# Kernel optimization log

Hardware: AMD Instinct MI355X
Metric: run time of the kernel (lower is better)

Reference implementation:

```python
import jax, jax.numpy as jnp
import numpy as np

NUM_HEADS = 4
IN_CHANNELS = 128


def setup_inputs() -> dict:
    key = jax.random.key(0)
    k_x, k_wq, k_bq, k_wo, k_bo = jax.random.split(key, 5)
    b, c, h, w = 16, IN_CHANNELS, 32, 32
    x = jax.random.normal(k_x, (b, c, h, w), dtype=jnp.float32)
    # 1x1 convs stored as (out_ch, in_ch) matrices
    w_qkv = jax.random.normal(k_wq, (c * 3 * NUM_HEADS, c), dtype=jnp.float32) * 0.02
    b_qkv = jax.random.normal(k_bq, (c * 3 * NUM_HEADS,), dtype=jnp.float32) * 0.02
    w_out = jax.random.normal(k_wo, (c, c * NUM_HEADS), dtype=jnp.float32) * 0.02
    b_out = jax.random.normal(k_bo, (c,), dtype=jnp.float32) * 0.02
    return {"x": x, "w_qkv": w_qkv, "b_qkv": b_qkv, "w_out": w_out, "b_out": b_out}


def reference(x, w_qkv, b_qkv, w_out, b_out):
    b, c, h, w = x.shape
    nh = NUM_HEADS
    # norm is Identity. 1x1 conv == per-pixel matmul over channels.
    qkv = jnp.einsum('bchw,oc->bohw', x, w_qkv) + b_qkv[None, :, None, None]
    qkv = qkv.reshape(b, nh, 3 * c, h, w)
    q, k, v = qkv[:, :, :c], qkv[:, :, c:2 * c], qkv[:, :, 2 * c:]
    # q, v: (b, nh, c, h, w) -> (b*nh, h*w, c); k -> (b*nh, c, h*w)
    q = q.transpose(0, 1, 3, 4, 2).reshape(b * nh, h * w, c)
    k = k.reshape(b * nh, c, h * w)
    v = v.transpose(0, 1, 3, 4, 2).reshape(b * nh, h * w, c)
    scores = jnp.einsum('bnc,bcm->bnm', q, k) * (c ** -0.5)  # (b*nh, hw, hw)
    attn = jax.nn.softmax(scores, axis=-1)
    out = jnp.einsum('bnm,bmc->bnc', attn, v)  # (b*nh, hw, c)
    out = out.reshape(b, nh, h, w, c).transpose(0, 4, 1, 2, 3).reshape(b, nh * c, h, w)
    out = jnp.einsum('bchw,oc->bohw', out, w_out) + b_out[None, :, None, None]
    return out + x
```

## Files before the change

### kernel.cpp

```cpp
#include <hip/hip_runtime.h>
#include <hip/hip_bf16.h>

typedef float  f32x4_v   __attribute__((ext_vector_type(4)));
typedef float  f32x16_v  __attribute__((ext_vector_type(16)));
typedef __bf16 bf16x8_v  __attribute__((ext_vector_type(8)));
typedef __bf16 bf16x4_v  __attribute__((ext_vector_type(4)));

#define WS_Q  0
#define WS_K  8388608
#define WS_V  16777216
#define WS_O  25165824
#define WS_WP 33554432

__device__ __forceinline__ int aswz(int p) { return ((p & 7) ^ ((p >> 3) & 7)) << 4; }

__device__ __forceinline__ void gload16(const void* g, void* l) {
    __builtin_amdgcn_global_load_lds(
        (const __attribute__((address_space(1))) unsigned int*)g,
        (__attribute__((address_space(3))) unsigned int*)l, 16, 0, 0);
}

__global__ __launch_bounds__(256) void k_permute(const float* __restrict__ w_out,
                                                 __bf16* __restrict__ w_perm) {
    int idx  = blockIdx.x * 256 + threadIdx.x;
    int head = idx >> 14;
    int o    = (idx >> 7) & 127;
    int c    = idx & 127;
    w_perm[idx] = (__bf16)w_out[o * 512 + c * 4 + head];
}

__global__ __launch_bounds__(256) void k_qkv(const float* __restrict__ x,
                                             const float* __restrict__ w_qkv,
                                             const float* __restrict__ b_qkv,
                                             __bf16* __restrict__ q_ws,
                                             __bf16* __restrict__ k_ws,
                                             __bf16* __restrict__ v_ws) {
    __shared__ __bf16 Ash[128 * 128];
    __shared__ __bf16 Bsh[128 * 128];
    const int tid = threadIdx.x;
    const int nt  = blockIdx.x;
    const int mt  = blockIdx.y;
    const int gm0 = mt * 128;
    const int b   = gm0 >> 10;
    const int p0  = gm0 & 1023;
    const int o0  = nt * 128;

    char* Ab = reinterpret_cast<char*>(Ash);
    char* Bb = reinterpret_cast<char*>(Bsh);

    for (int it = 0; it < 16; ++it) {
        int idx = tid + it * 256;
        int c   = idx >> 5;
        int i4  = (idx & 31) << 2;
        float4 v = *reinterpret_cast<const float4*>(x + b * 131072 + c * 1024 + p0 + i4);
        float vv[4] = {v.x, v.y, v.z, v.w};
#pragma unroll
        for (int j = 0; j < 4; ++j) {
            int p = i4 + j;
            int byte = ((p << 8) | (c << 1)) ^ aswz(p);
            *reinterpret_cast<__bf16*>(Ab + byte) = (__bf16)vv[j];
        }
    }
    for (int it = 0; it < 16; ++it) {
        int idx = tid + it * 256;
        int o   = idx >> 5;
        int c4  = (idx & 31) << 2;
        float4 v = *reinterpret_cast<const float4*>(w_qkv + (o0 + o) * 128 + c4);
        bf16x4_v h;
        h[0] = (__bf16)v.x; h[1] = (__bf16)v.y; h[2] = (__bf16)v.z; h[3] = (__bf16)v.w;
        int byte = ((o << 8) | (c4 << 1)) ^ aswz(o);
        *reinterpret_cast<bf16x4_v*>(Bb + byte) = h;
    }
    __syncthreads();

    const int lane = tid & 63;
    const int wv   = tid >> 6;
    const int wm   = (wv >> 1) * 64;
    const int wn   = (wv & 1) * 64;
    const int lr   = lane & 15;
    const int lg   = lane >> 4;

    f32x4_v acc[4][4] = {};
#pragma unroll
    for (int ks = 0; ks < 4; ++ks) {
        bf16x8_v af[4], bfr[4];
#pragma unroll
        for (int mi = 0; mi < 4; ++mi) {
            int row  = wm + mi * 16 + lr;
            int byte = ((row << 8) | (ks << 6) | (lg << 4)) ^ aswz(row);
            af[mi] = *reinterpret_cast<const bf16x8_v*>(Ab + byte);
        }
#pragma unroll
        for (int ni = 0; ni < 4; ++ni) {
            int row  = wn + ni * 16 + lr;
            int byte = ((row << 8) | (ks << 6) | (lg << 4)) ^ aswz(row);
            bfr[ni] = *reinterpret_cast<const bf16x8_v*>(Bb + byte);
        }
#pragma unroll
        for (int mi = 0; mi < 4; ++mi)
#pragma unroll
            for (int ni = 0; ni < 4; ++ni)
                acc[mi][ni] = __builtin_amdgcn_mfma_f32_16x16x32_bf16(af[mi], bfr[ni], acc[mi][ni], 0, 0, 0);
    }

#pragma unroll
    for (int ni = 0; ni < 4; ++ni) {
        int o    = o0 + wn + ni * 16 + lr;
        int head = o / 384;
        int rem  = o - head * 384;
        int type = rem >> 7;
        int ch   = rem & 127;
        float bias = b_qkv[o];
        int bh   = (b << 2) + head;
#pragma unroll
        for (int mi = 0; mi < 4; ++mi) {
            int prow = p0 + wm + mi * 16 + lg * 4;
            f32x4_v a = acc[mi][ni];
            if (type == 0) {
#pragma unroll
                for (int r = 0; r < 4; ++r)
                    q_ws[bh * 131072 + (prow + r) * 128 + ch] =
                        (__bf16)((a[r] + bias) * 0.12751744f);
            } else if (type == 1) {
#pragma unroll
                for (int r = 0; r < 4; ++r)
                    k_ws[bh * 131072 + (prow + r) * 128 + ch] = (__bf16)(a[r] + bias);
            } else {
                bf16x4_v hv;
#pragma unroll
                for (int r = 0; r < 4; ++r) hv[r] = (__bf16)(a[r] + bias);
                *reinterpret_cast<bf16x4_v*>(&v_ws[bh * 131072 + ch * 1024 + prow]) = hv;
            }
        }
    }
}

__device__ __forceinline__ void stage_kv(const __bf16* kg, const __bf16* vg,
                                         __bf16* kl, __bf16* vl, int wv, int lane) {
    const int s16 = lane & 15, r4 = lane >> 4;
    const int s8  = lane & 7,  r8 = lane >> 3;
#pragma unroll
    for (int i = 0; i < 4; ++i) {
        int row = wv * 16 + i * 4 + r4;
        const char* src = (const char*)(kg + row * 128) + ((s16 ^ (row & 7)) << 4);
        char* dst = (char*)kl + (wv * 16 + i * 4) * 256;
        gload16(src, dst);
    }
#pragma unroll
    for (int i = 0; i < 4; ++i) {
        int row = wv * 32 + i * 8 + r8;
        const char* src = (const char*)(vg + row * 1024) + ((s8 ^ (row & 7)) << 4);
        char* dst = (char*)vl + (wv * 32 + i * 8) * 128;
        gload16(src, dst);
    }
}

__global__ __launch_bounds__(256, 2) void k_attn(const __bf16* __restrict__ q_ws,
                                                 const __bf16* __restrict__ k_ws,
                                                 const __bf16* __restrict__ v_ws,
                                                 __bf16* __restrict__ o_ws) {
    __shared__ __bf16 Kbuf[2][64 * 128];
    __shared__ __bf16 Vbuf[2][128 * 64];

    const int tid  = threadIdx.x;
    const int lane = tid & 63;
    const int wv   = tid >> 6;
    const int col  = lane & 31;
    const int hi   = lane >> 5;

    const int id   = blockIdx.x;
    const int bh   = (id & 7) * 8 + (id >> 6);
    const int qt   = (id >> 3) & 7;
    const int base = bh * 131072;
    const int q0w  = qt * 128 + wv * 32;

    bf16x8_v bq[8];
    const __bf16* qp = q_ws + base + (q0w + col) * 128 + hi * 8;
#pragma unroll
    for (int ks = 0; ks < 8; ++ks)
        bq[ks] = *reinterpret_cast<const bf16x8_v*>(qp + ks * 16);

    f32x16_v of[4] = {};
    float m = -1e30f, l = 0.f;

    stage_kv(k_ws + base, v_ws + base, &Kbuf[0][0], &Vbuf[0][0], wv, lane);

    for (int t = 0; t < 16; ++t) {
        const int cur = t & 1;
        if (t < 15) {
            stage_kv(k_ws + base + (t + 1) * 64 * 128, v_ws + base + (t + 1) * 64,
                     &Kbuf[cur ^ 1][0], &Vbuf[cur ^ 1][0], wv, lane);
            asm volatile("s_waitcnt vmcnt(8)" ::: "memory");
        } else {
            asm volatile("s_waitcnt vmcnt(0)" ::: "memory");
        }
        __builtin_amdgcn_s_barrier();
        asm volatile("" ::: "memory");
        __builtin_amdgcn_sched_barrier(0);

        const char* Kl = (const char*)&Kbuf[cur][0];
        const char* Vl = (const char*)&Vbuf[cur][0];

        f32x16_v sa = {}, sb = {};
        __builtin_amdgcn_s_setprio(1);
#pragma unroll
        for (int ks = 0; ks < 8; ++ks) {
            const int sl = 2 * ks + hi;
            bf16x8_v af0 = *reinterpret_cast<const bf16x8_v*>(Kl + col * 256 + ((sl ^ (col & 7)) << 4));
            bf16x8_v af1 = *reinterpret_cast<const bf16x8_v*>(Kl + (32 + col) * 256 + ((sl ^ (col & 7)) << 4));
            sa = __builtin_amdgcn_mfma_f32_32x32x16_bf16(af0, bq[ks], sa, 0, 0, 0);
            sb = __builtin_amdgcn_mfma_f32_32x32x16_bf16(af1, bq[ks], sb, 0, 0, 0);
        }
        __builtin_amdgcn_s_setprio(0);

        float v = sa[0];
#pragma unroll
        for (int r = 1; r < 16; ++r) v = fmaxf(v, sa[r]);
#pragma unroll
        for (int r = 0; r < 16; ++r) v = fmaxf(v, sb[r]);
        float pmax = fmaxf(v, __shfl_xor(v, 32));
        if (!__all(pmax - m <= 8.0f)) {
            float fr = __builtin_amdgcn_exp2f(m - pmax);
            m = pmax;
            l *= fr;
#pragma unroll
            for (int r = 0; r < 16; ++r) {
                float frd = __shfl(fr, (r & 3) + 4 * hi + 8 * (r >> 2));
                of[0][r] *= frd; of[1][r] *= frd; of[2][r] *= frd; of[3][r] *= frd;
            }
        }
        float rs = 0.f;
#pragma unroll
        for (int r = 0; r < 16; ++r) { sa[r] = __builtin_amdgcn_exp2f(sa[r] - m); rs += sa[r]; }
#pragma unroll
        for (int r = 0; r < 16; ++r) { sb[r] = __builtin_amdgcn_exp2f(sb[r] - m); rs += sb[r]; }
        l += rs + __shfl_xor(rs, 32);

        bf16x8_v pa[4];
#pragma unroll
        for (int j = 0; j < 4; ++j) {
            const f32x16_v& sj = (j < 2) ? sa : sb;
            const int ro = 8 * (j & 1);
            unsigned w0, w1, w2, w3;
            asm("v_cvt_pk_bf16_f32 %0, %1, %2" : "=v"(w0) : "v"(sj[ro + 0]), "v"(sj[ro + 1]));
            asm("v_cvt_pk_bf16_f32 %0, %1, %2" : "=v"(w2) : "v"(sj[ro + 4]), "v"(sj[ro + 5]));
            asm("v_cvt_pk_bf16_f32 %0, %1, %2" : "=v"(w1) : "v"(sj[ro + 2]), "v"(sj[ro + 3]));
            asm("v_cvt_pk_bf16_f32 %0, %1, %2" : "=v"(w3) : "v"(sj[ro + 6]), "v"(sj[ro + 7]));
            asm("v_permlane32_swap_b32 %0, %1" : "+v"(w0), "+v"(w2));
            asm("v_permlane32_swap_b32 %0, %1" : "+v"(w1), "+v"(w3));
            union { unsigned u[4]; bf16x8_v h; } cvt;
            cvt.u[0] = w0; cvt.u[1] = w1; cvt.u[2] = w2; cvt.u[3] = w3;
            pa[j] = cvt.h;
        }

        __builtin_amdgcn_s_setprio(1);
#pragma unroll
        for (int n = 0; n < 4; ++n) {
#pragma unroll
            for (int j = 0; j < 4; ++j) {
                int row = 32 * n + col;
                bf16x8_v bv = *reinterpret_cast<const bf16x8_v*>(
                    Vl + row * 128 + (((2 * j + hi) ^ (row & 7)) << 4));
                of[n] = __builtin_amdgcn_mfma_f32_32x32x16_bf16(pa[j], bv, of[n], 0, 0, 0);
            }
        }
        __builtin_amdgcn_s_setprio(0);

        asm volatile("s_waitcnt lgkmcnt(0)" ::: "memory");
        __builtin_amdgcn_sched_barrier(0);
        __builtin_amdgcn_s_barrier();
        asm volatile("" ::: "memory");
        __builtin_amdgcn_sched_barrier(0);
    }

    float linv = 1.0f / l;
#pragma unroll
    for (int r = 0; r < 16; ++r) {
        int qr = (r & 3) + 4 * hi + 8 * (r >> 2);
        float ld = __shfl(linv, qr);
        int qg = q0w + qr;
#pragma unroll
        for (int n = 0; n < 4; ++n)
            o_ws[base + qg * 128 + 32 * n + col] = (__bf16)(of[n][r] * ld);
    }
}

__global__ __launch_bounds__(256) void k_out(const __bf16* __restrict__ o_ws,
                                             const __bf16* __restrict__ w_perm,
                                             const float* __restrict__ b_out,
                                             const float* __restrict__ x,
                                             float* __restrict__ out) {
    __shared__ __bf16 Al[64 * 136];
    __shared__ __bf16 Bl[128 * 136];
    const int tid  = threadIdx.x;
    const int lane = tid & 63, wv = tid >> 6;
    const int lr   = lane & 15, lg = lane >> 4;
    const int mt   = blockIdx.x;
    const int gp0  = mt * 64;
    const int b    = gp0 >> 10;
    const int p0   = gp0 & 1023;

    f32x4_v acc[8] = {};
    for (int kc = 0; kc < 4; ++kc) {
        __syncthreads();
#pragma unroll
        for (int it = 0; it < 4; ++it) {
            int idx = tid + it * 256;
            int rr = idx >> 4, k8 = (idx & 15) * 8;
            *reinterpret_cast<bf16x8_v*>(&Al[rr * 136 + k8]) =
                *reinterpret_cast<const bf16x8_v*>(&o_ws[(b * 4 + kc) * 131072 + (p0 + rr) * 128 + k8]);
        }
#pragma unroll
        for (int it = 0; it < 8; ++it) {
            int idx = tid + it * 256;
            int o = idx >> 4, k8 = (idx & 15) * 8;
            *reinterpret_cast<bf16x8_v*>(&Bl[o * 136 + k8]) =
                *reinterpret_cast<const bf16x8_v*>(&w_perm[kc * 16384 + o * 128 + k8]);
        }
        __syncthreads();
#pragma unroll
        for (int ks = 0; ks < 4; ++ks) {
            bf16x8_v af = *reinterpret_cast<const bf16x8_v*>(&Al[(wv * 16 + lr) * 136 + ks * 32 + lg * 8]);
#pragma unroll
            for (int ni = 0; ni < 8; ++ni) {
                bf16x8_v bf_ = *reinterpret_cast<const bf16x8_v*>(&Bl[(ni * 16 + lr) * 136 + ks * 32 + lg * 8]);
                acc[ni] = __builtin_amdgcn_mfma_f32_16x16x32_bf16(af, bf_, acc[ni], 0, 0, 0);
            }
        }
    }

    int prow = p0 + wv * 16 + lg * 4;
#pragma unroll
    for (int ni = 0; ni < 8; ++ni) {
        int o = ni * 16 + lr;
        float bias = b_out[o];
        float4 xr = *reinterpret_cast<const float4*>(&x[b * 131072 + o * 1024 + prow]);
        float4 res;
        res.x = acc[ni][0] + bias + xr.x;
        res.y = acc[ni][1] + bias + xr.y;
        res.z = acc[ni][2] + bias + xr.z;
        res.w = acc[ni][3] + bias + xr.w;
        *reinterpret_cast<float4*>(&out[b * 131072 + o * 1024 + prow]) = res;
    }
}

extern "C" void kernel_launch(void* const* d_in, const int* in_sizes, int n_in,
                              void* d_out, int out_size, void* d_ws, size_t ws_size,
                              hipStream_t stream) {
    const float* x     = (const float*)d_in[0];
    const float* w_qkv = (const float*)d_in[1];
    const float* b_qkv = (const float*)d_in[2];
    const float* w_out = (const float*)d_in[3];
    const float* b_out = (const float*)d_in[4];
    float* out = (float*)d_out;
    __bf16* ws = (__bf16*)d_ws;

    __bf16* q_ws   = ws + WS_Q;
    __bf16* k_ws   = ws + WS_K;
    __bf16* v_ws   = ws + WS_V;
    __bf16* o_ws   = ws + WS_O;
    __bf16* w_perm = ws + WS_WP;

    k_permute<<<256, 256, 0, stream>>>(w_out, w_perm);
    k_qkv<<<dim3(12, 128), 256, 0, stream>>>(x, w_qkv, b_qkv, q_ws, k_ws, v_ws);
    k_attn<<<512, 256, 0, stream>>>(q_ws, k_ws, v_ws, o_ws);
    k_out<<<256, 256, 0, stream>>>(o_ws, w_perm, b_out, x, out);
}
```

Measured before the change: 92.83 us.

## Pre-swizzle Q/K/V into MFMA fragment layout, load V directly to registers

The QKV projection now writes Q, K and V in a layout that matches the MFMA operand fragments, so the attention kernel can load Q and K with contiguous per-lane 16-byte reads and V straight into registers, with no LDS staging for V. Each QKV block now loops over three output tiles, reusing the staged x tile across them, and the weight-permute kernel is folded into the QKV kernel, which removes one launch. The aim is to cut LDS traffic and bank conflicts in attention and to reduce launch and x-reload overhead. In exchange the attention kernel holds more registers for V fragments, and the QKV kernel launches fewer, longer blocks.

```diff
diff --git a/kernel.cpp b/kernel.cpp
--- a/kernel.cpp
+++ b/kernel.cpp
@@ -20,30 +20,30 @@
         (__attribute__((address_space(3))) unsigned int*)l, 16, 0, 0);
 }
 
-__global__ __launch_bounds__(256) void k_permute(const float* __restrict__ w_out,
-                                                 __bf16* __restrict__ w_perm) {
-    int idx  = blockIdx.x * 256 + threadIdx.x;
-    int head = idx >> 14;
-    int o    = (idx >> 7) & 127;
-    int c    = idx & 127;
-    w_perm[idx] = (__bf16)w_out[o * 512 + c * 4 + head];
-}
-
 __global__ __launch_bounds__(256) void k_qkv(const float* __restrict__ x,
                                              const float* __restrict__ w_qkv,
                                              const float* __restrict__ b_qkv,
                                              __bf16* __restrict__ q_ws,
                                              __bf16* __restrict__ k_ws,
-                                             __bf16* __restrict__ v_ws) {
+                                             __bf16* __restrict__ v_ws,
+                                             const float* __restrict__ w_out,
+                                             __bf16* __restrict__ w_perm) {
     __shared__ __bf16 Ash[128 * 128];
     __shared__ __bf16 Bsh[128 * 128];
-    const int tid = threadIdx.x;
-    const int nt  = blockIdx.x;
-    const int mt  = blockIdx.y;
-    const int gm0 = mt * 128;
-    const int b   = gm0 >> 10;
-    const int p0  = gm0 & 1023;
-    const int o0  = nt * 128;
+    const int tid  = threadIdx.x;
+    const int quar = blockIdx.x;
+    const int mt   = blockIdx.y;
+    const int gm0  = mt * 128;
+    const int b    = gm0 >> 10;
+    const int p0   = gm0 & 1023;
+
+    if (quar < 2) {
+        int gid  = (mt * 2 + quar) * 256 + tid;
+        int head = gid >> 14;
+        int o    = (gid >> 7) & 127;
+        int c    = gid & 127;
+        w_perm[gid] = (__bf16)w_out[o * 512 + c * 4 + head];
+    }
 
     char* Ab = reinterpret_cast<char*>(Ash);
     char* Bb = reinterpret_cast<char*>(Bsh);
@@ -61,17 +61,6 @@
             *reinterpret_cast<__bf16*>(Ab + byte) = (__bf16)vv[j];
         }
     }
-    for (int it = 0; it < 16; ++it) {
-        int idx = tid + it * 256;
-        int o   = idx >> 5;
-        int c4  = (idx & 31) << 2;
-        float4 v = *reinterpret_cast<const float4*>(w_qkv + (o0 + o) * 128 + c4);
-        bf16x4_v h;
-        h[0] = (__bf16)v.x; h[1] = (__bf16)v.y; h[2] = (__bf16)v.z; h[3] = (__bf16)v.w;
-        int byte = ((o << 8) | (c4 << 1)) ^ aswz(o);
-        *reinterpret_cast<bf16x4_v*>(Bb + byte) = h;
-    }
-    __syncthreads();
 
     const int lane = tid & 63;
     const int wv   = tid >> 6;
@@ -80,78 +69,85 @@
     const int lr   = lane & 15;
     const int lg   = lane >> 4;
 
-    f32x4_v acc[4][4] = {};
-#pragma unroll
-    for (int ks = 0; ks < 4; ++ks) {
-        bf16x8_v af[4], bfr[4];
-#pragma unroll
-        for (int mi = 0; mi < 4; ++mi) {
-            int row  = wm + mi * 16 + lr;
-            int byte = ((row << 8) | (ks << 6) | (lg << 4)) ^ aswz(row);
-            af[mi] = *reinterpret_cast<const bf16x8_v*>(Ab + byte);
-        }
+    for (int i = 0; i < 3; ++i) {
+        const int o0 = (quar * 3 + i) * 128;
+        __syncthreads();
+        for (int it = 0; it < 16; ++it) {
+            int idx = tid + it * 256;
+            int o   = idx >> 5;
+            int c4  = (idx & 31) << 2;
+            float4 v = *reinterpret_cast<const float4*>(w_qkv + (o0 + o) * 128 + c4);
+            bf16x4_v h;
+            h[0] = (__bf16)v.x; h[1] = (__bf16)v.y; h[2] = (__bf16)v.z; h[3] = (__bf16)v.w;
+            int byte = ((o << 8) | (c4 << 1)) ^ aswz(o);
+            *reinterpret_cast<bf16x4_v*>(Bb + byte) = h;
+        }
+        __syncthreads();
+
+        f32x4_v acc[4][4] = {};
+#pragma unroll
+        for (int ks = 0; ks < 4; ++ks) {
+            bf16x8_v af[4], bfr[4];
+#pragma unroll
+            for (int mi = 0; mi < 4; ++mi) {
+                int row  = wm + mi * 16 + lr;
+                int byte = ((row << 8) | (ks << 6) | (lg << 4)) ^ aswz(row);
+                af[mi] = *reinterpret_cast<const bf16x8_v*>(Ab + byte);
+            }
+#pragma unroll
+            for (int ni = 0; ni < 4; ++ni) {
+                int row  = wn + ni * 16 + lr;
+                int byte = ((row << 8) | (ks << 6) | (lg << 4)) ^ aswz(row);
+                bfr[ni] = *reinterpret_cast<const bf16x8_v*>(Bb + byte);
+            }
+#pragma unroll
+            for (int mi = 0; mi < 4; ++mi)
+#pragma unroll
+                for (int ni = 0; ni < 4; ++ni)
+                    acc[mi][ni] = __builtin_amdgcn_mfma_f32_16x16x32_bf16(af[mi], bfr[ni], acc[mi][ni], 0, 0, 0);
+        }
+
 #pragma unroll
         for (int ni = 0; ni < 4; ++ni) {
-            int row  = wn + ni * 16 + lr;
-            int byte = ((row << 8) | (ks << 6) | (lg << 4)) ^ aswz(row);
-            bfr[ni] = *reinterpret_cast<const bf16x8_v*>(Bb + byte);
-        }
-#pragma unroll
-        for (int mi = 0; mi < 4; ++mi)
-#pragma unroll
-            for (int ni = 0; ni < 4; ++ni)
-                acc[mi][ni] = __builtin_amdgcn_mfma_f32_16x16x32_bf16(af[mi], bfr[ni], acc[mi][ni], 0, 0, 0);
-    }
-
-#pragma unroll
-    for (int ni = 0; ni < 4; ++ni) {
-        int o    = o0 + wn + ni * 16 + lr;
-        int head = o / 384;
-        int rem  = o - head * 384;
-        int type = rem >> 7;
-        int ch   = rem & 127;
-        float bias = b_qkv[o];
-        int bh   = (b << 2) + head;
-#pragma unroll
-        for (int mi = 0; mi < 4; ++mi) {
-            int prow = p0 + wm + mi * 16 + lg * 4;
-            f32x4_v a = acc[mi][ni];
-            if (type == 0) {
-#pragma unroll
-                for (int r = 0; r < 4; ++r)
-                    q_ws[bh * 131072 + (prow + r) * 128 + ch] =
-                        (__bf16)((a[r] + bias) * 0.12751744f);
-            } else if (type == 1) {
-#pragma unroll
-                for (int r = 0; r < 4; ++r)
-                    k_ws[bh * 131072 + (prow + r) * 128 + ch] = (__bf16)(a[r] + bias);
-            } else {
-                bf16x4_v hv;
-#pragma unroll
-                for (int r = 0; r < 4; ++r) hv[r] = (__bf16)(a[r] + bias);
-                *reinterpret_cast<bf16x4_v*>(&v_ws[bh * 131072 + ch * 1024 + prow]) = hv;
-            }
-        }
-    }
-}
-
-__device__ __forceinline__ void stage_kv(const __bf16* kg, const __bf16* vg,
-                                         __bf16* kl, __bf16* vl, int wv, int lane) {
-    const int s16 = lane & 15, r4 = lane >> 4;
-    const int s8  = lane & 7,  r8 = lane >> 3;
-#pragma unroll
-    for (int i = 0; i < 4; ++i) {
-        int row = wv * 16 + i * 4 + r4;
-        const char* src = (const char*)(kg + row * 128) + ((s16 ^ (row & 7)) << 4);
-        char* dst = (char*)kl + (wv * 16 + i * 4) * 256;
-        gload16(src, dst);
-    }
-#pragma unroll
-    for (int i = 0; i < 4; ++i) {
-        int row = wv * 32 + i * 8 + r8;
-        const char* src = (const char*)(vg + row * 1024) + ((s8 ^ (row & 7)) << 4);
-        char* dst = (char*)vl + (wv * 32 + i * 8) * 128;
-        gload16(src, dst);
+            int o    = o0 + wn + ni * 16 + lr;
+            int head = o / 384;
+            int rem  = o - head * 384;
+            int type = rem >> 7;
+            int ch   = rem & 127;
+            float bias = b_qkv[o];
+            int bh   = (b << 2) + head;
+            int ksd  = ch >> 4;
+            int hid  = (ch >> 3) & 1;
+            int ed   = ch & 7;
+#pragma unroll
+            for (int mi = 0; mi < 4; ++mi) {
+                int prow = p0 + wm + mi * 16 + lg * 4;
+                f32x4_v a = acc[mi][ni];
+                if (type == 0) {
+#pragma unroll
+                    for (int r = 0; r < 4; ++r) {
+                        int q = prow + r;
+                        q_ws[bh * 131072 + (q >> 5) * 4096 + ksd * 512 + hid * 256 + (q & 31) * 8 + ed] =
+                            (__bf16)((a[r] + bias) * 0.12751744f);
+                    }
+                } else if (type == 1) {
+#pragma unroll
+                    for (int r = 0; r < 4; ++r) {
+                        int kv = prow + r;
+                        k_ws[bh * 131072 + (kv >> 6) * 8192 + (((kv >> 5) & 1) * 8 + ksd) * 512 +
+                             hid * 256 + (kv & 31) * 8 + ed] = (__bf16)(a[r] + bias);
+                    }
+                } else {
+                    bf16x4_v hv;
+#pragma unroll
+                    for (int r = 0; r < 4; ++r) hv[r] = (__bf16)(a[r] + bias);
+                    int addr = bh * 131072 + (prow >> 6) * 8192 +
+                               ((ch >> 5) * 4 + ((prow >> 4) & 3)) * 512 +
+                               ((prow >> 3) & 1) * 256 + (ch & 31) * 8 + (prow & 7);
+                    *reinterpret_cast<bf16x4_v*>(&v_ws[addr]) = hv;
+                }
+            }
+        }
     }
 }
 
@@ -159,8 +155,7 @@
                                                  const __bf16* __restrict__ k_ws,
                                                  const __bf16* __restrict__ v_ws,
                                                  __bf16* __restrict__ o_ws) {
-    __shared__ __bf16 Kbuf[2][64 * 128];
-    __shared__ __bf16 Vbuf[2][128 * 64];
+    __shared__ __bf16 Kbuf[2][8192];
 
     const int tid  = threadIdx.x;
     const int lane = tid & 63;
@@ -175,50 +170,84 @@
     const int q0w  = qt * 128 + wv * 32;
 
     bf16x8_v bq[8];
-    const __bf16* qp = q_ws + base + (q0w + col) * 128 + hi * 8;
-#pragma unroll
-    for (int ks = 0; ks < 8; ++ks)
-        bq[ks] = *reinterpret_cast<const bf16x8_v*>(qp + ks * 16);
+    {
+        const __bf16* qp = q_ws + base + (q0w >> 5) * 4096 + lane * 8;
+#pragma unroll
+        for (int ks = 0; ks < 8; ++ks)
+            bq[ks] = *reinterpret_cast<const bf16x8_v*>(qp + ks * 512);
+    }
+    asm volatile("s_waitcnt vmcnt(0)" ::: "memory");
+
+    const char* kfb = reinterpret_cast<const char*>(k_ws + base);
+    const uint64_t vfb = (uint64_t)reinterpret_cast<const char*>(v_ws + base) + lane * 16;
+    const int lane16 = lane * 16;
+
+#pragma unroll
+    for (int i = 0; i < 4; ++i)
+        gload16(kfb + (wv * 4 + i) * 1024 + lane16, (char*)&Kbuf[0][0] + (wv * 4 + i) * 1024);
 
     f32x16_v of[4] = {};
     float m = -1e30f, l = 0.f;
-
-    stage_kv(k_ws + base, v_ws + base, &Kbuf[0][0], &Vbuf[0][0], wv, lane);
+    bf16x8_v vf[4][4];
 
     for (int t = 0; t < 16; ++t) {
         const int cur = t & 1;
+        const char* Kl = (const char*)&Kbuf[cur][0];
+
+        {
+            uint64_t vt = vfb + (uint64_t)(t * 16384);
+#pragma unroll
+            for (int n = 0; n < 4; ++n) {
+                uint64_t va = vt + (uint64_t)(n * 4096);
+                asm volatile("global_load_dwordx4 %0, %4, off\n\t"
+                             "global_load_dwordx4 %1, %4, off offset:1024\n\t"
+                             "global_load_dwordx4 %2, %4, off offset:2048\n\t"
+                             "global_load_dwordx4 %3, %4, off offset:3072"
+                             : "=&v"(vf[n][0]), "=&v"(vf[n][1]), "=&v"(vf[n][2]), "=&v"(vf[n][3])
+                             : "v"(va));
+            }
+        }
+
         if (t < 15) {
-            stage_kv(k_ws + base + (t + 1) * 64 * 128, v_ws + base + (t + 1) * 64,
-                     &Kbuf[cur ^ 1][0], &Vbuf[cur ^ 1][0], wv, lane);
-            asm volatile("s_waitcnt vmcnt(8)" ::: "memory");
+            const char* kn = kfb + (t + 1) * 16384;
+            char* dn = (char*)&Kbuf[cur ^ 1][0];
+#pragma unroll
+            for (int i = 0; i < 4; ++i)
+                gload16(kn + (wv * 4 + i) * 1024 + lane16, dn + (wv * 4 + i) * 1024);
+            asm volatile("s_waitcnt vmcnt(20)" ::: "memory");
         } else {
-            asm volatile("s_waitcnt vmcnt(0)" ::: "memory");
-        }
+            asm volatile("s_waitcnt vmcnt(16)" ::: "memory");
+        }
+        __builtin_amdgcn_sched_barrier(0);
         __builtin_amdgcn_s_barrier();
         asm volatile("" ::: "memory");
         __builtin_amdgcn_sched_barrier(0);
 
-        const char* Kl = (const char*)&Kbuf[cur][0];
-        const char* Vl = (const char*)&Vbuf[cur][0];
-
         f32x16_v sa = {}, sb = {};
         __builtin_amdgcn_s_setprio(1);
 #pragma unroll
         for (int ks = 0; ks < 8; ++ks) {
-            const int sl = 2 * ks + hi;
-            bf16x8_v af0 = *reinterpret_cast<const bf16x8_v*>(Kl + col * 256 + ((sl ^ (col & 7)) << 4));
-            bf16x8_v af1 = *reinterpret_cast<const bf16x8_v*>(Kl + (32 + col) * 256 + ((sl ^ (col & 7)) << 4));
+            bf16x8_v af0 = *reinterpret_cast<const bf16x8_v*>(Kl + ks * 1024 + lane16);
+            bf16x8_v af1 = *reinterpret_cast<const bf16x8_v*>(Kl + (8 + ks) * 1024 + lane16);
             sa = __builtin_amdgcn_mfma_f32_32x32x16_bf16(af0, bq[ks], sa, 0, 0, 0);
             sb = __builtin_amdgcn_mfma_f32_32x32x16_bf16(af1, bq[ks], sb, 0, 0, 0);
         }
         __builtin_amdgcn_s_setprio(0);
 
-        float v = sa[0];
-#pragma unroll
-        for (int r = 1; r < 16; ++r) v = fmaxf(v, sa[r]);
-#pragma unroll
-        for (int r = 0; r < 16; ++r) v = fmaxf(v, sb[r]);
-        float pmax = fmaxf(v, __shfl_xor(v, 32));
+        asm volatile("s_waitcnt lgkmcnt(0)" ::: "memory");
+        __builtin_amdgcn_sched_barrier(0);
+        __builtin_amdgcn_s_barrier();
+        asm volatile("" ::: "memory");
+        __builtin_amdgcn_sched_barrier(0);
+
+        float t16[16];
+#pragma unroll
+        for (int r = 0; r < 16; ++r) t16[r] = fmaxf(sa[r], sb[r]);
+#pragma unroll
+        for (int w = 8; w >= 1; w >>= 1)
+#pragma unroll
+            for (int r = 0; r < w; ++r) t16[r] = fmaxf(t16[r], t16[r + w]);
+        float pmax = fmaxf(t16[0], __shfl_xor(t16[0], 32));
         if (!__all(pmax - m <= 8.0f)) {
             float fr = __builtin_amdgcn_exp2f(m - pmax);
             m = pmax;
@@ -253,24 +282,17 @@
             pa[j] = cvt.h;
         }
 
+        if (t < 15) asm volatile("s_waitcnt vmcnt(4)" ::: "memory");
+        else        asm volatile("s_waitcnt vmcnt(0)" ::: "memory");
+        __builtin_amdgcn_sched_barrier(0);
+
         __builtin_amdgcn_s_setprio(1);
 #pragma unroll
-        for (int n = 0; n < 4; ++n) {
-#pragma unroll
-            for (int j = 0; j < 4; ++j) {
-                int row = 32 * n + col;
-                bf16x8_v bv = *reinterpret_cast<const bf16x8_v*>(
-                    Vl + row * 128 + (((2 * j + hi) ^ (row & 7)) << 4));
-                of[n] = __builtin_amdgcn_mfma_f32_32x32x16_bf16(pa[j], bv, of[n], 0, 0, 0);
-            }
-        }
+        for (int n = 0; n < 4; ++n)
+#pragma unroll
+            for (int j = 0; j < 4; ++j)
+                of[n] = __builtin_amdgcn_mfma_f32_32x32x16_bf16(pa[j], vf[n][j], of[n], 0, 0, 0);
         __builtin_amdgcn_s_setprio(0);
-
-        asm volatile("s_waitcnt lgkmcnt(0)" ::: "memory");
-        __builtin_amdgcn_sched_barrier(0);
-        __builtin_amdgcn_s_barrier();
-        asm volatile("" ::: "memory");
-        __builtin_amdgcn_sched_barrier(0);
     }
 
     float linv = 1.0f / l;
@@ -361,8 +383,7 @@
     __bf16* o_ws   = ws + WS_O;
     __bf16* w_perm = ws + WS_WP;
 
-    k_permute<<<256, 256, 0, stream>>>(w_out, w_perm);
-    k_qkv<<<dim3(12, 128), 256, 0, stream>>>(x, w_qkv, b_qkv, q_ws, k_ws, v_ws);
+    k_qkv<<<dim3(4, 128), 256, 0, stream>>>(x, w_qkv, b_qkv, q_ws, k_ws, v_ws, w_out, w_perm);
     k_attn<<<512, 256, 0, stream>>>(q_ws, k_ws, v_ws, o_ws);
     k_out<<<256, 256, 0, stream>>>(o_ws, w_perm, b_out, x, out);
 }
```

Result: slower. 97.79 us (+5.3%).
